# Kernel optimization log

Measured on AMD Instinct MI355X. Metric: run time of the kernel, lower is better.

Reference implementation:

```python
import jax, jax.numpy as jnp
import numpy as np

N_NODES = 50000
N_EDGES = 800000
IN_DIM = 64
EDGE_DIM = 16
HID = 128
L = 3
G = 128  # number of graphs in the batch
EPS = 1e-5


def _glorot(key, shape):
    fan_in, fan_out = shape[0], shape[1]
    lim = float(np.sqrt(6.0 / (fan_in + fan_out)))
    return jax.random.uniform(key, shape, jnp.float32, -lim, lim)


def setup_inputs() -> dict:
    key = jax.random.key(0)
    ks = jax.random.split(key, 40)
    inp = {}
    inp["x"] = jax.random.uniform(ks[0], (N_NODES, IN_DIM), jnp.float32)
    inp["edge_index"] = jax.random.randint(ks[1], (2, N_EDGES), 0, N_NODES, jnp.int64)
    inp["edge_attr"] = jax.random.normal(ks[2], (N_EDGES, EDGE_DIM), jnp.float32)
    inp["batch"] = jnp.sort(jax.random.randint(ks[3], (N_NODES,), 0, G, jnp.int64))
    # ligand / protein input MLPs: Linear-ReLU-Linear-ReLU
    inp["lig_w1"] = _glorot(ks[4], (IN_DIM, HID)); inp["lig_b1"] = jnp.zeros((HID,), jnp.float32)
    inp["lig_w2"] = _glorot(ks[5], (HID, HID));    inp["lig_b2"] = jnp.zeros((HID,), jnp.float32)
    inp["prot_w1"] = _glorot(ks[6], (IN_DIM, HID)); inp["prot_b1"] = jnp.zeros((HID,), jnp.float32)
    inp["prot_w2"] = _glorot(ks[7], (HID, HID));    inp["prot_b2"] = jnp.zeros((HID,), jnp.float32)
    # per-layer GINEConv params (stacked over layers)
    inp["edge_w"] = jnp.stack([_glorot(ks[8 + i], (EDGE_DIM, HID)) for i in range(L)])
    inp["edge_b"] = jnp.zeros((L, HID), jnp.float32)
    inp["nn_w1"] = jnp.stack([_glorot(ks[12 + i], (HID, HID)) for i in range(L)])
    inp["nn_b1"] = jnp.zeros((L, HID), jnp.float32)
    inp["nn_w2"] = jnp.stack([_glorot(ks[16 + i], (HID, HID)) for i in range(L)])
    inp["nn_b2"] = jnp.zeros((L, HID), jnp.float32)
    # GraphNorm params: weight=1, bias=0, mean_scale=1
    inp["gn_w"] = jnp.ones((L, HID), jnp.float32)
    inp["gn_b"] = jnp.zeros((L, HID), jnp.float32)
    inp["gn_ms"] = jnp.ones((L, HID), jnp.float32)
    # output head: Linear-ReLU-Linear(1)
    inp["fc_w1"] = _glorot(ks[20], (HID, HID)); inp["fc_b1"] = jnp.zeros((HID,), jnp.float32)
    inp["fc_w2"] = _glorot(ks[21], (HID, 1));   inp["fc_b2"] = jnp.zeros((1,), jnp.float32)
    return inp


def reference(x, edge_index, edge_attr, batch,
              lig_w1, lig_b1, lig_w2, lig_b2,
              prot_w1, prot_b1, prot_w2, prot_b2,
              edge_w, edge_b, nn_w1, nn_b1, nn_w2, nn_b2,
              gn_w, gn_b, gn_ms,
              fc_w1, fc_b1, fc_w2, fc_b2):
    relu = lambda a: jnp.maximum(a, 0)
    src, dst = edge_index[0], edge_index[1]

    # input encoders, merged per node by protein flag (last feature column)
    is_prot = x[:, -1] > 0.5
    h_lig = relu(relu(x @ lig_w1 + lig_b1) @ lig_w2 + lig_b2)
    h_prot = relu(relu(x @ prot_w1 + prot_b1) @ prot_w2 + prot_b2)
    h = jnp.where(is_prot[:, None], h_prot, h_lig)

    # per-graph node counts for GraphNorm
    cnt = jax.ops.segment_sum(jnp.ones((x.shape[0],), jnp.float32), batch, num_segments=G)
    cnt = jnp.maximum(cnt, 1.0)[:, None]

    for l in range(L):
        # GINEConv (eps=0): out = nn(x + sum_{j->i} relu(x_j + lin(e_ji)))
        e = edge_attr @ edge_w[l] + edge_b[l]              # [E, HID]
        msg = relu(h[src] + e)                             # gather + add + relu
        aggr = jax.ops.segment_sum(msg, dst, num_segments=h.shape[0])
        h = aggr + h
        h = relu(h @ nn_w1[l] + nn_b1[l]) @ nn_w2[l] + nn_b2[l]
        # GraphNorm: per-graph mean/var with learnable mean_scale
        mean = jax.ops.segment_sum(h, batch, num_segments=G) / cnt
        hc = h - mean[batch] * gn_ms[l]
        var = jax.ops.segment_sum(hc * hc, batch, num_segments=G) / cnt
        h = gn_w[l] * hc * jax.lax.rsqrt(var[batch] + EPS) + gn_b[l]
        h = relu(h)  # (dropout=0.0 -> identity)

    g = jax.ops.segment_sum(h, batch, num_segments=G)      # global_add_pool
    out = relu(g @ fc_w1 + fc_b1) @ fc_w2 + fc_b2
    return out.reshape(-1)
```

## Files before the change

### kernel.cpp

```cpp
#include <hip/hip_runtime.h>

#define N_NODES 50000
#define N_EDGES 800000
#define IN_DIM  64
#define EDGE_DIM 16
#define HID     128
#define NLAYERS 3
#define NGRAPH  128
#define EPS     1e-5f

typedef __attribute__((ext_vector_type(8))) short bf8_t;
typedef __attribute__((ext_vector_type(4))) short bf4_t;
typedef __attribute__((ext_vector_type(4))) float f32x4;

__device__ __forceinline__ unsigned short f2bf(float x) {
    unsigned u = __float_as_uint(x);
    unsigned r = u + 0x7fffu + ((u >> 16) & 1u);
    return (unsigned short)(r >> 16);
}
__device__ __forceinline__ float bf2f(unsigned short v) {
    return __uint_as_float(((unsigned)v) << 16);
}

__global__ void k_init(int* __restrict__ row_cnt, float* __restrict__ pool,
                       float* __restrict__ gsum, float* __restrict__ gsq) {
    int i = blockIdx.x * blockDim.x + threadIdx.x;
    if (i < N_NODES) row_cnt[i] = 0;
    if (i < NGRAPH * HID) { pool[i] = 0.0f; gsum[i] = 0.0f; gsq[i] = 0.0f; }
}

__global__ __launch_bounds__(NGRAPH) void k_count(const int* __restrict__ batch,
                                                  float* __restrict__ cnt) {
    int g = threadIdx.x;
    int lo = 0, hi = N_NODES;
    while (lo < hi) { int mid = (lo + hi) >> 1; if (batch[mid] < g) lo = mid + 1; else hi = mid; }
    int a = lo;
    lo = 0; hi = N_NODES;
    while (lo < hi) { int mid = (lo + hi) >> 1; if (batch[mid] < g + 1) lo = mid + 1; else hi = mid; }
    cnt[g] = (float)(lo - a);
}

__global__ void k_wconv(const float* __restrict__ nw1, const float* __restrict__ nw2,
                        unsigned short* __restrict__ wt) {
    int idx = blockIdx.x * 256 + threadIdx.x;
    if (idx >= NLAYERS * 2 * HID * HID) return;
    int k = idx & 127;
    int n = (idx >> 7) & 127;
    int which = (idx >> 14) & 1;
    int l = idx >> 15;
    const float* w = (which == 0 ? nw1 : nw2) + l * HID * HID;
    wt[idx] = f2bf(w[k * HID + n]);
}

__global__ void k_wconv_enc(const float* __restrict__ lw1, const float* __restrict__ pw1,
                            const float* __restrict__ lw2, const float* __restrict__ pw2,
                            unsigned short* __restrict__ we) {
    int idx = blockIdx.x * 256 + threadIdx.x;
    if (idx >= 49152) return;
    float v;
    if (idx < 8192)       { int n = idx >> 6, k = idx & 63;            v = lw1[k * HID + n]; }
    else if (idx < 16384) { int r = idx - 8192;  int n = r >> 6, k = r & 63;  v = pw1[k * HID + n]; }
    else if (idx < 32768) { int r = idx - 16384; int n = r >> 7, k = r & 127; v = lw2[k * HID + n]; }
    else                  { int r = idx - 32768; int n = r >> 7, k = r & 127; v = pw2[k * HID + n]; }
    we[idx] = f2bf(v);
}

__global__ void k_wconv_e(const float* __restrict__ ew, const float* __restrict__ eb,
                          unsigned short* __restrict__ wte) {
    int idx = blockIdx.x * 256 + threadIdx.x;
    if (idx >= NLAYERS * 8 * 64 * 8) return;
    int j = idx & 7;
    int lane = (idx >> 3) & 63;
    int t = (idx >> 9) & 7;
    int l = idx >> 12;
    int k = (lane >> 4) * 8 + j;
    int feat = t * 16 + (lane & 15);
    float v = 0.0f;
    if (k < EDGE_DIM)       v = ew[l * EDGE_DIM * HID + k * HID + feat];
    else if (k == EDGE_DIM) v = eb[l * HID + feat];
    wte[idx] = f2bf(v);
}

__global__ void k_hist(const int* __restrict__ dsts, int* __restrict__ row_cnt) {
    int e = blockIdx.x * blockDim.x + threadIdx.x;
    if (e < N_EDGES) atomicAdd(&row_cnt[dsts[e]], 1);
}

__global__ __launch_bounds__(256) void k_scan1(const int* __restrict__ row_cnt,
                                               int* __restrict__ partial) {
    __shared__ int s[256];
    int t = threadIdx.x, b = blockIdx.x;
    int i0 = b * 512 + t;
    int v = 0;
    if (i0 < N_NODES) v += row_cnt[i0];
    if (i0 + 256 < N_NODES) v += row_cnt[i0 + 256];
    s[t] = v; __syncthreads();
    for (int off = 128; off > 0; off >>= 1) {
        if (t < off) s[t] += s[t + off];
        __syncthreads();
    }
    if (t == 0) partial[b] = s[0];
}

#define NCHUNK 98
__global__ __launch_bounds__(128) void k_scan2(int* __restrict__ partial) {
    __shared__ int s[128];
    int t = threadIdx.x;
    int v = (t < NCHUNK) ? partial[t] : 0;
    s[t] = v; __syncthreads();
    for (int off = 1; off < 128; off <<= 1) {
        int x = (t >= off) ? s[t - off] : 0;
        __syncthreads();
        s[t] += x;
        __syncthreads();
    }
    partial[t] = s[t] - v;
}

__global__ __launch_bounds__(512) void k_scan3(const int* __restrict__ row_cnt,
                                               const int* __restrict__ partial,
                                               int* __restrict__ row_start,
                                               int* __restrict__ row_fill) {
    __shared__ int s[512];
    int t = threadIdx.x, b = blockIdx.x;
    int i = b * 512 + t;
    int v = (i < N_NODES) ? row_cnt[i] : 0;
    s[t] = v; __syncthreads();
    for (int off = 1; off < 512; off <<= 1) {
        int x = (t >= off) ? s[t - off] : 0;
        __syncthreads();
        s[t] += x;
        __syncthreads();
    }
    int excl = s[t] - v + partial[b];
    if (i < N_NODES) { row_start[i] = excl; row_fill[i] = excl; }
}

__global__ void k_fill(const int* __restrict__ srcs, const int* __restrict__ dsts,
                       int* __restrict__ row_fill, int2* __restrict__ csr_se) {
    int e = blockIdx.x * blockDim.x + threadIdx.x;
    if (e < N_EDGES) {
        int p = atomicAdd(&row_fill[dsts[e]], 1);
        csr_se[p] = make_int2(srcs[e], e);
    }
}

__global__ __launch_bounds__(256) void k_reorder(const int2* __restrict__ csr_se,
                                                 const float* __restrict__ ea,
                                                 int* __restrict__ csr_src,
                                                 unsigned short* __restrict__ cea) {
    int p = blockIdx.x * blockDim.x + threadIdx.x;
    if (p < N_EDGES) {
        int2 se = csr_se[p];
        csr_src[p] = se.x;
        const float* s = ea + (size_t)se.y * EDGE_DIM;
        float4 a0 = *(const float4*)(s);
        float4 a1 = *(const float4*)(s + 4);
        float4 a2 = *(const float4*)(s + 8);
        float4 a3 = *(const float4*)(s + 12);
        bf8_t v0, v1;
        v0[0] = (short)f2bf(a0.x); v0[1] = (short)f2bf(a0.y);
        v0[2] = (short)f2bf(a0.z); v0[3] = (short)f2bf(a0.w);
        v0[4] = (short)f2bf(a1.x); v0[5] = (short)f2bf(a1.y);
        v0[6] = (short)f2bf(a1.z); v0[7] = (short)f2bf(a1.w);
        v1[0] = (short)f2bf(a2.x); v1[1] = (short)f2bf(a2.y);
        v1[2] = (short)f2bf(a2.z); v1[3] = (short)f2bf(a2.w);
        v1[4] = (short)f2bf(a3.x); v1[5] = (short)f2bf(a3.y);
        v1[6] = (short)f2bf(a3.z); v1[7] = (short)f2bf(a3.w);
        *(bf8_t*)(cea + (size_t)p * EDGE_DIM) = v0;
        *(bf8_t*)(cea + (size_t)p * EDGE_DIM + 8) = v1;
    }
}

#define HS 136
__global__ __launch_bounds__(256, 8) void k_encoder_mfma(
    const float* __restrict__ x,
    const unsigned short* __restrict__ we,
    const float* __restrict__ lb1, const float* __restrict__ lb2,
    const float* __restrict__ pb1, const float* __restrict__ pb2,
    unsigned short* __restrict__ Hbp) {
    __shared__ short h1s[4][16 * HS];
    int w = threadIdx.x >> 6, lane = threadIdx.x & 63;
    int m = lane & 15, quad = lane >> 4;
    int tile = w >> 1, role = w & 1;
    int nb = blockIdx.x * 32 + tile * 16;
    short* hl = h1s[w];
    int nclamp = nb + m; if (nclamp >= N_NODES) nclamp = N_NODES - 1;
    const float* xp = x + (size_t)nclamp * IN_DIM;
    const float* b1 = role ? pb1 : lb1;
    const float* b2 = role ? pb2 : lb2;
    const unsigned short* w1 = we + role * 8192;
    const unsigned short* w2 = we + 16384 + role * 16384;

    f32x4 a1[8];
    #pragma unroll
    for (int t = 0; t < 8; ++t) {
        float bv = b1[t * 16 + m];
        a1[t] = (f32x4){bv, bv, bv, bv};
    }
    #pragma unroll
    for (int s_ = 0; s_ < 2; ++s_) {
        int k0 = s_ * 32 + quad * 8;
        float4 a0 = *(const float4*)(xp + k0);
        float4 a1v = *(const float4*)(xp + k0 + 4);
        bf8_t af;
        af[0] = (short)f2bf(a0.x); af[1] = (short)f2bf(a0.y);
        af[2] = (short)f2bf(a0.z); af[3] = (short)f2bf(a0.w);
        af[4] = (short)f2bf(a1v.x); af[5] = (short)f2bf(a1v.y);
        af[6] = (short)f2bf(a1v.z); af[7] = (short)f2bf(a1v.w);
        #pragma unroll
        for (int t = 0; t < 8; ++t) {
            bf8_t bw = *(const bf8_t*)(w1 + (t * 16 + m) * 64 + k0);
            a1[t] = __builtin_amdgcn_mfma_f32_16x16x32_bf16(af, bw, a1[t], 0, 0, 0);
        }
    }
    #pragma unroll
    for (int t = 0; t < 8; ++t)
        #pragma unroll
        for (int r = 0; r < 4; ++r)
            hl[(quad * 4 + r) * HS + t * 16 + m] = (short)f2bf(fmaxf(a1[t][r], 0.0f));
    __syncthreads();
    f32x4 a2[8];
    #pragma unroll
    for (int t = 0; t < 8; ++t) {
        float bv = b2[t * 16 + m];
        a2[t] = (f32x4){bv, bv, bv, bv};
    }
    #pragma unroll
    for (int s_ = 0; s_ < 4; ++s_) {
        int k0 = s_ * 32 + quad * 8;
        bf8_t af = *(const bf8_t*)(hl + m * HS + k0);
        #pragma unroll
        for (int t = 0; t < 8; ++t) {
            bf8_t bw = *(const bf8_t*)(w2 + (t * 16 + m) * 128 + k0);
            a2[t] = __builtin_amdgcn_mfma_f32_16x16x32_bf16(af, bw, a2[t], 0, 0, 0);
        }
    }
    #pragma unroll
    for (int r = 0; r < 4; ++r) {
        int node = nb + quad * 4 + r;
        if (node < N_NODES) {
            bool prot = x[(size_t)node * IN_DIM + (IN_DIM - 1)] > 0.5f;
            if (prot == (role == 1)) {
                bf8_t o;
                #pragma unroll
                for (int t = 0; t < 8; ++t)
                    o[t] = (short)f2bf(fmaxf(a2[t][r], 0.0f));
                *(bf8_t*)(Hbp + (size_t)node * HID + m * 8) = o;
            }
        }
    }
}

__global__ __launch_bounds__(256, 8) void k_gather(
    const int* __restrict__ csr_src, const unsigned short* __restrict__ cea,
    const int* __restrict__ row_start, const int* __restrict__ row_end,
    const unsigned short* __restrict__ wte,
    const unsigned short* __restrict__ Hbp, unsigned short* __restrict__ Abp) {
    int w = threadIdx.x >> 6, lane = threadIdx.x & 63;
    int m = lane & 15, quad = lane >> 4;
    int n = blockIdx.x * 2 + (w >> 1);
    int half = w & 1;

    bf8_t bw[4];
    #pragma unroll
    for (int t = 0; t < 4; ++t)
        bw[t] = *(const bf8_t*)(wte + ((size_t)(half * 4 + t) * 64 + lane) * 8);

    float acc[4];
    #pragma unroll
    for (int t = 0; t < 4; ++t) acc[t] = 0.0f;

    int p  = __builtin_amdgcn_readfirstlane(row_start[n]);
    int pe = __builtin_amdgcn_readfirstlane(row_end[n]);

    const f32x4 zc = (f32x4){0.0f, 0.0f, 0.0f, 0.0f};

    for (; p + 16 <= pe; p += 16) {
        bf8_t af = (bf8_t){0, 0, 0, 0, 0, 0, 0, 0};
        if (quad < 2)
            af = *(const bf8_t*)(cea + (size_t)(p + m) * EDGE_DIM + quad * 8);
        else if (quad == 2)
            af[0] = (short)0x3F80;
        int sr[4];
        #pragma unroll
        for (int r = 0; r < 4; ++r) sr[r] = csr_src[p + quad * 4 + r];
        bf4_t hrow[4];
        #pragma unroll
        for (int r = 0; r < 4; ++r)
            hrow[r] = *(const bf4_t*)(Hbp + (size_t)sr[r] * HID + m * 8 + half * 4);
        f32x4 d[4];
        #pragma unroll
        for (int t = 0; t < 4; ++t)
            d[t] = __builtin_amdgcn_mfma_f32_16x16x32_bf16(af, bw[t], zc, 0, 0, 0);
        #pragma unroll
        for (int t = 0; t < 4; ++t)
            #pragma unroll
            for (int r = 0; r < 4; ++r)
                acc[t] += fmaxf(bf2f((unsigned short)hrow[r][t]) + d[t][r], 0.0f);
    }
    int rem = pe - p;
    if (rem > 0) {
        bf8_t af = (bf8_t){0, 0, 0, 0, 0, 0, 0, 0};
        if (quad < 2 && m < rem)
            af = *(const bf8_t*)(cea + (size_t)(p + m) * EDGE_DIM + quad * 8);
        else if (quad == 2)
            af[0] = (short)0x3F80;
        int sr[4];
        #pragma unroll
        for (int r = 0; r < 4; ++r) {
            int idx = p + quad * 4 + r; if (idx >= pe) idx = pe - 1;
            sr[r] = csr_src[idx];
        }
        bf4_t hrow[4];
        #pragma unroll
        for (int r = 0; r < 4; ++r)
            hrow[r] = *(const bf4_t*)(Hbp + (size_t)sr[r] * HID + m * 8 + half * 4);
        f32x4 d[4];
        #pragma unroll
        for (int t = 0; t < 4; ++t)
            d[t] = __builtin_amdgcn_mfma_f32_16x16x32_bf16(af, bw[t], zc, 0, 0, 0);
        #pragma unroll
        for (int t = 0; t < 4; ++t)
            #pragma unroll
            for (int r = 0; r < 4; ++r)
                if (quad * 4 + r < rem)
                    acc[t] += fmaxf(bf2f((unsigned short)hrow[r][t]) + d[t][r], 0.0f);
    }
    #pragma unroll
    for (int t = 0; t < 4; ++t) {
        acc[t] += __shfl_xor(acc[t], 16);
        acc[t] += __shfl_xor(acc[t], 32);
    }
    float asel = (quad == 0) ? acc[0] : (quad == 1) ? acc[1] : (quad == 2) ? acc[2] : acc[3];
    float self_ = bf2f(Hbp[(size_t)n * HID + m * 8 + half * 4 + quad]);
    Abp[(size_t)n * HID + (half * 4 + quad) * 16 + m] = f2bf(asel + self_);
}

#define MLP_NODES_PER_BLOCK 32
__global__ __launch_bounds__(256, 6) void k_mlp_mfma(
    const unsigned short* __restrict__ Abp, const int* __restrict__ batch,
    const unsigned short* __restrict__ wt1, const unsigned short* __restrict__ wt2,
    const float* __restrict__ b1, const float* __restrict__ b2,
    unsigned short* __restrict__ Hb, float* __restrict__ gsum, float* __restrict__ gsq) {
    __shared__ short h1s[2][16 * HS];
    int w = threadIdx.x >> 6;
    int lane = threadIdx.x & 63;
    int m = lane & 15;
    int quad = lane >> 4;
    int tile = w >> 1, role = w & 1;
    int nb = blockIdx.x * MLP_NODES_PER_BLOCK + tile * 16;
    short* hw = h1s[tile];
    int fbase = role * 64;

    int nclamp = nb + m; if (nclamp >= N_NODES) nclamp = N_NODES - 1;
    const unsigned short* Ap = Abp + (size_t)nclamp * HID;
    f32x4 acc1[4];
    #pragma unroll
    for (int t = 0; t < 4; ++t) {
        float bv = b1[fbase + t * 16 + m];
        acc1[t] = (f32x4){bv, bv, bv, bv};
    }
    #pragma unroll
    for (int s_ = 0; s_ < 4; ++s_) {
        int k0 = s_ * 32 + quad * 8;
        bf8_t af = *(const bf8_t*)(Ap + k0);
        #pragma unroll
        for (int t = 0; t < 4; ++t) {
            bf8_t bf = *(const bf8_t*)(wt1 + (size_t)(fbase + t * 16 + m) * HID + k0);
            acc1[t] = __builtin_amdgcn_mfma_f32_16x16x32_bf16(af, bf, acc1[t], 0, 0, 0);
        }
    }
    #pragma unroll
    for (int t = 0; t < 4; ++t)
        #pragma unroll
        for (int r = 0; r < 4; ++r) {
            float v = fmaxf(acc1[t][r], 0.0f);
            hw[(quad * 4 + r) * HS + fbase + t * 16 + m] = (short)f2bf(v);
        }
    __syncthreads();
    f32x4 acc2[4];
    #pragma unroll
    for (int t = 0; t < 4; ++t) {
        float bv = b2[fbase + t * 16 + m];
        acc2[t] = (f32x4){bv, bv, bv, bv};
    }
    #pragma unroll
    for (int s_ = 0; s_ < 4; ++s_) {
        int k0 = s_ * 32 + quad * 8;
        bf8_t af = *(const bf8_t*)(hw + m * HS + k0);
        #pragma unroll
        for (int t = 0; t < 4; ++t) {
            bf8_t bf = *(const bf8_t*)(wt2 + (size_t)(fbase + t * 16 + m) * HID + k0);
            acc2[t] = __builtin_amdgcn_mfma_f32_16x16x32_bf16(af, bf, acc2[t], 0, 0, 0);
        }
    }
    #pragma unroll
    for (int t = 0; t < 4; ++t)
        #pragma unroll
        for (int r = 0; r < 4; ++r) {
            int node = nb + quad * 4 + r;
            if (node < N_NODES) Hb[(size_t)node * HID + fbase + t * 16 + m] = f2bf(acc2[t][r]);
        }
    int blast = nb + 15 < N_NODES ? batch[nb + 15] : -1;
    int g0 = batch[nb < N_NODES ? nb : N_NODES - 1];
    if (nb + 15 < N_NODES && g0 == blast) {
        #pragma unroll
        for (int t = 0; t < 4; ++t) {
            float s = 0.0f, q = 0.0f;
            #pragma unroll
            for (int r = 0; r < 4; ++r) { float v = acc2[t][r]; s += v; q += v * v; }
            s += __shfl_xor(s, 16); q += __shfl_xor(q, 16);
            s += __shfl_xor(s, 32); q += __shfl_xor(q, 32);
            if (quad == 0) {
                atomicAdd(&gsum[g0 * HID + fbase + t * 16 + m], s);
                atomicAdd(&gsq[g0 * HID + fbase + t * 16 + m], q);
            }
        }
    } else {
        #pragma unroll
        for (int t = 0; t < 4; ++t)
            #pragma unroll
            for (int r = 0; r < 4; ++r) {
                int node = nb + quad * 4 + r;
                if (node < N_NODES) {
                    int g = batch[node];
                    float v = acc2[t][r];
                    atomicAdd(&gsum[g * HID + fbase + t * 16 + m], v);
                    atomicAdd(&gsq[g * HID + fbase + t * 16 + m], v * v);
                }
            }
    }
}

__global__ __launch_bounds__(HID) void k_stats(
    float* __restrict__ gsum, float* __restrict__ gsq,
    const float* __restrict__ cnt,
    const float* __restrict__ gw, const float* __restrict__ gb,
    const float* __restrict__ gms,
    float* __restrict__ sc, float* __restrict__ of) {
    int g = blockIdx.x;
    int t = threadIdx.x;
    float c = fmaxf(cnt[g], 1.0f);
    float mean = gsum[g * HID + t] / c;
    float msq  = gsq[g * HID + t] / c;
    float ms = gms[t];
    float var = msq - mean * mean * ms * (2.0f - ms);
    var = fmaxf(var, 0.0f);
    float istd = rsqrtf(var + EPS);
    float s = gw[t] * istd;
    sc[g * HID + t] = s;
    of[g * HID + t] = gb[t] - s * mean * ms;
    gsum[g * HID + t] = 0.0f;
    gsq[g * HID + t]  = 0.0f;
}

#define NORM_N 8
__global__ __launch_bounds__(HID) void k_norm(
    const unsigned short* __restrict__ Hb, const int* __restrict__ batch,
    const float* __restrict__ sc, const float* __restrict__ of,
    unsigned short* __restrict__ Hbp, float* __restrict__ pool, int accumulate) {
    int n0 = blockIdx.x * NORM_N;
    int t = threadIdx.x;
    int m = t & 15, tt = t >> 4;
    int g0 = batch[n0], gN = batch[n0 + NORM_N - 1];
    if (g0 == gN) {
        float ssc = sc[g0 * HID + t], sof = of[g0 * HID + t];
        float ps = 0.0f;
        #pragma unroll
        for (int i = 0; i < NORM_N; ++i) {
            float v = fmaxf(bf2f(Hb[(size_t)(n0 + i) * HID + t]) * ssc + sof, 0.0f);
            Hbp[(size_t)(n0 + i) * HID + m * 8 + tt] = f2bf(v);
            ps += v;
        }
        if (accumulate) atomicAdd(&pool[g0 * HID + t], ps);
    } else {
        #pragma unroll
        for (int i = 0; i < NORM_N; ++i) {
            int g = batch[n0 + i];
            float v = fmaxf(bf2f(Hb[(size_t)(n0 + i) * HID + t]) * sc[g * HID + t] + of[g * HID + t], 0.0f);
            Hbp[(size_t)(n0 + i) * HID + m * 8 + tt] = f2bf(v);
            if (accumulate) atomicAdd(&pool[g * HID + t], v);
        }
    }
}

__global__ __launch_bounds__(HID) void k_head(
    const float* __restrict__ pool,
    const float* __restrict__ fw1, const float* __restrict__ fb1,
    const float* __restrict__ fw2, const float* __restrict__ fb2,
    float* __restrict__ out) {
    __shared__ float ps[HID];
    __shared__ float red[2];
    int g = blockIdx.x;
    int t = threadIdx.x;
    ps[t] = pool[g * HID + t];
    __syncthreads();
    float acc = fb1[t];
    #pragma unroll 4
    for (int k = 0; k < HID; ++k) acc = fmaf(ps[k], fw1[k * HID + t], acc);
    float p = fmaxf(acc, 0.0f) * fw2[t];
    #pragma unroll
    for (int off = 32; off > 0; off >>= 1) p += __shfl_down(p, off, 64);
    if ((t & 63) == 0) red[t >> 6] = p;
    __syncthreads();
    if (t == 0) out[g] = red[0] + red[1] + fb2[0];
}

extern "C" void kernel_launch(void* const* d_in, const int* in_sizes, int n_in,
                              void* d_out, int out_size, void* d_ws, size_t ws_size,
                              hipStream_t stream) {
    const float* x     = (const float*)d_in[0];
    const int*   ei    = (const int*)d_in[1];
    const float* ea    = (const float*)d_in[2];
    const int*   batch = (const int*)d_in[3];
    const float* lw1 = (const float*)d_in[4];
    const float* lb1 = (const float*)d_in[5];
    const float* lw2 = (const float*)d_in[6];
    const float* lb2 = (const float*)d_in[7];
    const float* pw1 = (const float*)d_in[8];
    const float* pb1 = (const float*)d_in[9];
    const float* pw2 = (const float*)d_in[10];
    const float* pb2 = (const float*)d_in[11];
    const float* ew  = (const float*)d_in[12];
    const float* eb  = (const float*)d_in[13];
    const float* nw1 = (const float*)d_in[14];
    const float* nb1 = (const float*)d_in[15];
    const float* nw2 = (const float*)d_in[16];
    const float* nb2 = (const float*)d_in[17];
    const float* gw  = (const float*)d_in[18];
    const float* gb  = (const float*)d_in[19];
    const float* gms = (const float*)d_in[20];
    const float* fw1 = (const float*)d_in[21];
    const float* fb1 = (const float*)d_in[22];
    const float* fw2 = (const float*)d_in[23];
    const float* fb2 = (const float*)d_in[24];
    float* out = (float*)d_out;

    float* ws   = (float*)d_ws;
    float* H    = ws;
    float* A    = H    + (size_t)N_NODES * HID;
    float* gsum = A    + (size_t)N_NODES * HID;
    float* gsq  = gsum + NGRAPH * HID;
    float* sc   = gsq  + NGRAPH * HID;
    float* of   = sc   + NGRAPH * HID;
    float* pool = of   + NGRAPH * HID;
    float* cnt  = pool + NGRAPH * HID;
    int* row_cnt   = (int*)(cnt + NGRAPH);
    int* row_start = row_cnt + N_NODES;
    int* row_fill  = row_start + N_NODES;
    int* partial   = row_fill + N_NODES;
    int* csr_src   = partial + 128;
    unsigned short* cea  = (unsigned short*)(csr_src + N_EDGES);
    unsigned short* wt   = cea + (size_t)N_EDGES * EDGE_DIM;
    unsigned short* wenc = wt + NLAYERS * 2 * HID * HID;
    unsigned short* wte  = wenc + 49152;
    unsigned short* Hbp  = wte + NLAYERS * 8 * 64 * 8;
    unsigned short* Hb   = (unsigned short*)H;
    unsigned short* Abp  = (unsigned short*)A;
    int2* csr_se = (int2*)(Abp + (size_t)N_NODES * HID);

    const int* srcs = ei;
    const int* dsts = ei + N_EDGES;

    k_init<<<(N_NODES + 255) / 256, 256, 0, stream>>>(row_cnt, pool, gsum, gsq);
    k_count<<<1, NGRAPH, 0, stream>>>(batch, cnt);
    k_wconv<<<(NLAYERS * 2 * HID * HID + 255) / 256, 256, 0, stream>>>(nw1, nw2, wt);
    k_wconv_enc<<<(49152 + 255) / 256, 256, 0, stream>>>(lw1, pw1, lw2, pw2, wenc);
    k_wconv_e<<<(NLAYERS * 8 * 64 * 8 + 255) / 256, 256, 0, stream>>>(ew, eb, wte);
    k_hist<<<(N_EDGES + 255) / 256, 256, 0, stream>>>(dsts, row_cnt);
    k_scan1<<<NCHUNK, 256, 0, stream>>>(row_cnt, partial);
    k_scan2<<<1, 128, 0, stream>>>(partial);
    k_scan3<<<NCHUNK, 512, 0, stream>>>(row_cnt, partial, row_start, row_fill);
    k_fill<<<(N_EDGES + 255) / 256, 256, 0, stream>>>(srcs, dsts, row_fill, csr_se);
    k_reorder<<<(N_EDGES + 255) / 256, 256, 0, stream>>>(csr_se, ea, csr_src, cea);

    k_encoder_mfma<<<(N_NODES + 31) / 32, 256, 0, stream>>>(
        x, wenc, lb1, lb2, pb1, pb2, Hbp);

    int mlp_blocks = (N_NODES + MLP_NODES_PER_BLOCK - 1) / MLP_NODES_PER_BLOCK;
    for (int l = 0; l < NLAYERS; ++l) {
        k_gather<<<N_NODES / 2, 256, 0, stream>>>(
            csr_src, cea, row_start, row_fill,
            wte + (size_t)l * 4096, Hbp, Abp);
        k_mlp_mfma<<<mlp_blocks, 256, 0, stream>>>(
            Abp, batch,
            wt + (size_t)l * 2 * HID * HID,
            wt + (size_t)l * 2 * HID * HID + HID * HID,
            nb1 + l * HID, nb2 + l * HID, Hb, gsum, gsq);
        k_stats<<<NGRAPH, HID, 0, stream>>>(gsum, gsq, cnt,
                                            gw + l * HID, gb + l * HID, gms + l * HID,
                                            sc, of);
        k_norm<<<N_NODES / NORM_N, HID, 0, stream>>>(
            Hb, batch, sc, of, Hbp, pool, (l == NLAYERS - 1) ? 1 : 0);
    }
    k_head<<<NGRAPH, HID, 0, stream>>>(pool, fw1, fb1, fw2, fb2, out);
}
```

Baseline: 659.2 us.

## Fuse edge gather with node MLP and fold GraphNorm stats into norm kernel

Merges the per-layer gather kernel and the two-layer MLP kernel into one kernel. It processes 16 nodes per block, keeps the aggregated features in shared memory instead of writing and re-reading an Abp buffer, and splits the MLP output columns across four waves. The separate stats kernel is removed. Per-layer gsum/gsq buffers are zeroed once up front, and k_norm recomputes scale and offset inline. This cuts global traffic and two launches per layer, but each block now runs 8 serial gather tasks per wave, so per-block latency and load imbalance may increase.

```diff
diff --git a/kernel.cpp b/kernel.cpp
--- a/kernel.cpp
+++ b/kernel.cpp
@@ -26,7 +26,8 @@
                        float* __restrict__ gsum, float* __restrict__ gsq) {
     int i = blockIdx.x * blockDim.x + threadIdx.x;
     if (i < N_NODES) row_cnt[i] = 0;
-    if (i < NGRAPH * HID) { pool[i] = 0.0f; gsum[i] = 0.0f; gsq[i] = 0.0f; }
+    if (i < NGRAPH * HID) pool[i] = 0.0f;
+    if (i < NLAYERS * NGRAPH * HID) { gsum[i] = 0.0f; gsq[i] = 0.0f; }
 }
 
 __global__ __launch_bounds__(NGRAPH) void k_count(const int* __restrict__ batch,
@@ -252,161 +253,150 @@
     }
 }
 
-__global__ __launch_bounds__(256, 8) void k_gather(
+#define GM_NODES 16
+__global__ __launch_bounds__(256, 8) void k_gm(
     const int* __restrict__ csr_src, const unsigned short* __restrict__ cea,
     const int* __restrict__ row_start, const int* __restrict__ row_end,
     const unsigned short* __restrict__ wte,
-    const unsigned short* __restrict__ Hbp, unsigned short* __restrict__ Abp) {
-    int w = threadIdx.x >> 6, lane = threadIdx.x & 63;
-    int m = lane & 15, quad = lane >> 4;
-    int n = blockIdx.x * 2 + (w >> 1);
-    int half = w & 1;
-
-    bf8_t bw[4];
-    #pragma unroll
-    for (int t = 0; t < 4; ++t)
-        bw[t] = *(const bf8_t*)(wte + ((size_t)(half * 4 + t) * 64 + lane) * 8);
-
-    float acc[4];
-    #pragma unroll
-    for (int t = 0; t < 4; ++t) acc[t] = 0.0f;
-
-    int p  = __builtin_amdgcn_readfirstlane(row_start[n]);
-    int pe = __builtin_amdgcn_readfirstlane(row_end[n]);
-
-    const f32x4 zc = (f32x4){0.0f, 0.0f, 0.0f, 0.0f};
-
-    for (; p + 16 <= pe; p += 16) {
-        bf8_t af = (bf8_t){0, 0, 0, 0, 0, 0, 0, 0};
-        if (quad < 2)
-            af = *(const bf8_t*)(cea + (size_t)(p + m) * EDGE_DIM + quad * 8);
-        else if (quad == 2)
-            af[0] = (short)0x3F80;
-        int sr[4];
-        #pragma unroll
-        for (int r = 0; r < 4; ++r) sr[r] = csr_src[p + quad * 4 + r];
-        bf4_t hrow[4];
-        #pragma unroll
-        for (int r = 0; r < 4; ++r)
-            hrow[r] = *(const bf4_t*)(Hbp + (size_t)sr[r] * HID + m * 8 + half * 4);
-        f32x4 d[4];
-        #pragma unroll
-        for (int t = 0; t < 4; ++t)
-            d[t] = __builtin_amdgcn_mfma_f32_16x16x32_bf16(af, bw[t], zc, 0, 0, 0);
-        #pragma unroll
-        for (int t = 0; t < 4; ++t)
-            #pragma unroll
-            for (int r = 0; r < 4; ++r)
-                acc[t] += fmaxf(bf2f((unsigned short)hrow[r][t]) + d[t][r], 0.0f);
-    }
-    int rem = pe - p;
-    if (rem > 0) {
-        bf8_t af = (bf8_t){0, 0, 0, 0, 0, 0, 0, 0};
-        if (quad < 2 && m < rem)
-            af = *(const bf8_t*)(cea + (size_t)(p + m) * EDGE_DIM + quad * 8);
-        else if (quad == 2)
-            af[0] = (short)0x3F80;
-        int sr[4];
-        #pragma unroll
-        for (int r = 0; r < 4; ++r) {
-            int idx = p + quad * 4 + r; if (idx >= pe) idx = pe - 1;
-            sr[r] = csr_src[idx];
-        }
-        bf4_t hrow[4];
-        #pragma unroll
-        for (int r = 0; r < 4; ++r)
-            hrow[r] = *(const bf4_t*)(Hbp + (size_t)sr[r] * HID + m * 8 + half * 4);
-        f32x4 d[4];
-        #pragma unroll
-        for (int t = 0; t < 4; ++t)
-            d[t] = __builtin_amdgcn_mfma_f32_16x16x32_bf16(af, bw[t], zc, 0, 0, 0);
-        #pragma unroll
-        for (int t = 0; t < 4; ++t)
-            #pragma unroll
-            for (int r = 0; r < 4; ++r)
-                if (quad * 4 + r < rem)
-                    acc[t] += fmaxf(bf2f((unsigned short)hrow[r][t]) + d[t][r], 0.0f);
-    }
-    #pragma unroll
-    for (int t = 0; t < 4; ++t) {
-        acc[t] += __shfl_xor(acc[t], 16);
-        acc[t] += __shfl_xor(acc[t], 32);
-    }
-    float asel = (quad == 0) ? acc[0] : (quad == 1) ? acc[1] : (quad == 2) ? acc[2] : acc[3];
-    float self_ = bf2f(Hbp[(size_t)n * HID + m * 8 + half * 4 + quad]);
-    Abp[(size_t)n * HID + (half * 4 + quad) * 16 + m] = f2bf(asel + self_);
-}
-
-#define MLP_NODES_PER_BLOCK 32
-__global__ __launch_bounds__(256, 6) void k_mlp_mfma(
-    const unsigned short* __restrict__ Abp, const int* __restrict__ batch,
+    const unsigned short* __restrict__ Hbp, const int* __restrict__ batch,
     const unsigned short* __restrict__ wt1, const unsigned short* __restrict__ wt2,
     const float* __restrict__ b1, const float* __restrict__ b2,
     unsigned short* __restrict__ Hb, float* __restrict__ gsum, float* __restrict__ gsq) {
-    __shared__ short h1s[2][16 * HS];
-    int w = threadIdx.x >> 6;
-    int lane = threadIdx.x & 63;
-    int m = lane & 15;
-    int quad = lane >> 4;
-    int tile = w >> 1, role = w & 1;
-    int nb = blockIdx.x * MLP_NODES_PER_BLOCK + tile * 16;
-    short* hw = h1s[tile];
-    int fbase = role * 64;
-
-    int nclamp = nb + m; if (nclamp >= N_NODES) nclamp = N_NODES - 1;
-    const unsigned short* Ap = Abp + (size_t)nclamp * HID;
-    f32x4 acc1[4];
-    #pragma unroll
-    for (int t = 0; t < 4; ++t) {
+    __shared__ short Als[GM_NODES * HS];
+    __shared__ short h1s[GM_NODES * HS];
+    int w = threadIdx.x >> 6, lane = threadIdx.x & 63;
+    int m = lane & 15, quad = lane >> 4;
+    int nb = blockIdx.x * GM_NODES;
+
+    const f32x4 zc = (f32x4){0.0f, 0.0f, 0.0f, 0.0f};
+
+    for (int task = 0; task < 8; ++task) {
+        int nl = w * 4 + (task >> 1);
+        int half = task & 1;
+        int n = nb + nl;
+
+        bf8_t bw[4];
+        #pragma unroll
+        for (int t = 0; t < 4; ++t)
+            bw[t] = *(const bf8_t*)(wte + ((size_t)(half * 4 + t) * 64 + lane) * 8);
+
+        float acc[4];
+        #pragma unroll
+        for (int t = 0; t < 4; ++t) acc[t] = 0.0f;
+
+        int p  = __builtin_amdgcn_readfirstlane(row_start[n]);
+        int pe = __builtin_amdgcn_readfirstlane(row_end[n]);
+
+        for (; p + 16 <= pe; p += 16) {
+            bf8_t af = (bf8_t){0, 0, 0, 0, 0, 0, 0, 0};
+            if (quad < 2)
+                af = *(const bf8_t*)(cea + (size_t)(p + m) * EDGE_DIM + quad * 8);
+            else if (quad == 2)
+                af[0] = (short)0x3F80;
+            int sr[4];
+            #pragma unroll
+            for (int r = 0; r < 4; ++r) sr[r] = csr_src[p + quad * 4 + r];
+            bf4_t hrow[4];
+            #pragma unroll
+            for (int r = 0; r < 4; ++r)
+                hrow[r] = *(const bf4_t*)(Hbp + (size_t)sr[r] * HID + m * 8 + half * 4);
+            #pragma unroll
+            for (int t = 0; t < 4; ++t) {
+                f32x4 d = __builtin_amdgcn_mfma_f32_16x16x32_bf16(af, bw[t], zc, 0, 0, 0);
+                #pragma unroll
+                for (int r = 0; r < 4; ++r)
+                    acc[t] += fmaxf(bf2f((unsigned short)hrow[r][t]) + d[r], 0.0f);
+            }
+        }
+        int rem = pe - p;
+        if (rem > 0) {
+            bf8_t af = (bf8_t){0, 0, 0, 0, 0, 0, 0, 0};
+            if (quad < 2 && m < rem)
+                af = *(const bf8_t*)(cea + (size_t)(p + m) * EDGE_DIM + quad * 8);
+            else if (quad == 2)
+                af[0] = (short)0x3F80;
+            int sr[4];
+            #pragma unroll
+            for (int r = 0; r < 4; ++r) {
+                int idx = p + quad * 4 + r; if (idx >= pe) idx = pe - 1;
+                sr[r] = csr_src[idx];
+            }
+            bf4_t hrow[4];
+            #pragma unroll
+            for (int r = 0; r < 4; ++r)
+                hrow[r] = *(const bf4_t*)(Hbp + (size_t)sr[r] * HID + m * 8 + half * 4);
+            #pragma unroll
+            for (int t = 0; t < 4; ++t) {
+                f32x4 d = __builtin_amdgcn_mfma_f32_16x16x32_bf16(af, bw[t], zc, 0, 0, 0);
+                #pragma unroll
+                for (int r = 0; r < 4; ++r)
+                    if (quad * 4 + r < rem)
+                        acc[t] += fmaxf(bf2f((unsigned short)hrow[r][t]) + d[r], 0.0f);
+            }
+        }
+        #pragma unroll
+        for (int t = 0; t < 4; ++t) {
+            acc[t] += __shfl_xor(acc[t], 16);
+            acc[t] += __shfl_xor(acc[t], 32);
+        }
+        float asel = (quad == 0) ? acc[0] : (quad == 1) ? acc[1] : (quad == 2) ? acc[2] : acc[3];
+        float self_ = bf2f(Hbp[(size_t)n * HID + m * 8 + half * 4 + quad]);
+        Als[nl * HS + (half * 4 + quad) * 16 + m] = (short)f2bf(asel + self_);
+    }
+    __syncthreads();
+
+    int fbase = w * 32;
+    f32x4 acc1[2];
+    #pragma unroll
+    for (int t = 0; t < 2; ++t) {
         float bv = b1[fbase + t * 16 + m];
         acc1[t] = (f32x4){bv, bv, bv, bv};
     }
     #pragma unroll
     for (int s_ = 0; s_ < 4; ++s_) {
         int k0 = s_ * 32 + quad * 8;
-        bf8_t af = *(const bf8_t*)(Ap + k0);
-        #pragma unroll
-        for (int t = 0; t < 4; ++t) {
+        bf8_t af = *(const bf8_t*)(Als + m * HS + k0);
+        #pragma unroll
+        for (int t = 0; t < 2; ++t) {
             bf8_t bf = *(const bf8_t*)(wt1 + (size_t)(fbase + t * 16 + m) * HID + k0);
             acc1[t] = __builtin_amdgcn_mfma_f32_16x16x32_bf16(af, bf, acc1[t], 0, 0, 0);
         }
     }
     #pragma unroll
-    for (int t = 0; t < 4; ++t)
+    for (int t = 0; t < 2; ++t)
         #pragma unroll
         for (int r = 0; r < 4; ++r) {
             float v = fmaxf(acc1[t][r], 0.0f);
-            hw[(quad * 4 + r) * HS + fbase + t * 16 + m] = (short)f2bf(v);
+            h1s[(quad * 4 + r) * HS + fbase + t * 16 + m] = (short)f2bf(v);
         }
     __syncthreads();
-    f32x4 acc2[4];
-    #pragma unroll
-    for (int t = 0; t < 4; ++t) {
+    f32x4 acc2[2];
+    #pragma unroll
+    for (int t = 0; t < 2; ++t) {
         float bv = b2[fbase + t * 16 + m];
         acc2[t] = (f32x4){bv, bv, bv, bv};
     }
     #pragma unroll
     for (int s_ = 0; s_ < 4; ++s_) {
         int k0 = s_ * 32 + quad * 8;
-        bf8_t af = *(const bf8_t*)(hw + m * HS + k0);
-        #pragma unroll
-        for (int t = 0; t < 4; ++t) {
+        bf8_t af = *(const bf8_t*)(h1s + m * HS + k0);
+        #pragma unroll
+        for (int t = 0; t < 2; ++t) {
             bf8_t bf = *(const bf8_t*)(wt2 + (size_t)(fbase + t * 16 + m) * HID + k0);
             acc2[t] = __builtin_amdgcn_mfma_f32_16x16x32_bf16(af, bf, acc2[t], 0, 0, 0);
         }
     }
     #pragma unroll
-    for (int t = 0; t < 4; ++t)
+    for (int t = 0; t < 2; ++t)
         #pragma unroll
         for (int r = 0; r < 4; ++r) {
             int node = nb + quad * 4 + r;
-            if (node < N_NODES) Hb[(size_t)node * HID + fbase + t * 16 + m] = f2bf(acc2[t][r]);
-        }
-    int blast = nb + 15 < N_NODES ? batch[nb + 15] : -1;
-    int g0 = batch[nb < N_NODES ? nb : N_NODES - 1];
-    if (nb + 15 < N_NODES && g0 == blast) {
-        #pragma unroll
-        for (int t = 0; t < 4; ++t) {
+            Hb[(size_t)node * HID + fbase + t * 16 + m] = f2bf(acc2[t][r]);
+        }
+    int g0 = batch[nb];
+    if (batch[nb + 15] == g0) {
+        #pragma unroll
+        for (int t = 0; t < 2; ++t) {
             float s = 0.0f, q = 0.0f;
             #pragma unroll
             for (int r = 0; r < 4; ++r) { float v = acc2[t][r]; s += v; q += v * v; }
@@ -419,53 +409,38 @@
         }
     } else {
         #pragma unroll
-        for (int t = 0; t < 4; ++t)
+        for (int t = 0; t < 2; ++t)
             #pragma unroll
             for (int r = 0; r < 4; ++r) {
                 int node = nb + quad * 4 + r;
-                if (node < N_NODES) {
-                    int g = batch[node];
-                    float v = acc2[t][r];
-                    atomicAdd(&gsum[g * HID + fbase + t * 16 + m], v);
-                    atomicAdd(&gsq[g * HID + fbase + t * 16 + m], v * v);
-                }
+                int g = batch[node];
+                float v = acc2[t][r];
+                atomicAdd(&gsum[g * HID + fbase + t * 16 + m], v);
+                atomicAdd(&gsq[g * HID + fbase + t * 16 + m], v * v);
             }
     }
 }
 
-__global__ __launch_bounds__(HID) void k_stats(
-    float* __restrict__ gsum, float* __restrict__ gsq,
+#define NORM_N 8
+__global__ __launch_bounds__(HID) void k_norm(
+    const unsigned short* __restrict__ Hb, const int* __restrict__ batch,
+    const float* __restrict__ gsum, const float* __restrict__ gsq,
     const float* __restrict__ cnt,
     const float* __restrict__ gw, const float* __restrict__ gb,
     const float* __restrict__ gms,
-    float* __restrict__ sc, float* __restrict__ of) {
-    int g = blockIdx.x;
-    int t = threadIdx.x;
-    float c = fmaxf(cnt[g], 1.0f);
-    float mean = gsum[g * HID + t] / c;
-    float msq  = gsq[g * HID + t] / c;
-    float ms = gms[t];
-    float var = msq - mean * mean * ms * (2.0f - ms);
-    var = fmaxf(var, 0.0f);
-    float istd = rsqrtf(var + EPS);
-    float s = gw[t] * istd;
-    sc[g * HID + t] = s;
-    of[g * HID + t] = gb[t] - s * mean * ms;
-    gsum[g * HID + t] = 0.0f;
-    gsq[g * HID + t]  = 0.0f;
-}
-
-#define NORM_N 8
-__global__ __launch_bounds__(HID) void k_norm(
-    const unsigned short* __restrict__ Hb, const int* __restrict__ batch,
-    const float* __restrict__ sc, const float* __restrict__ of,
     unsigned short* __restrict__ Hbp, float* __restrict__ pool, int accumulate) {
     int n0 = blockIdx.x * NORM_N;
     int t = threadIdx.x;
     int m = t & 15, tt = t >> 4;
+    float ms = gms[t], gwt = gw[t], gbt = gb[t];
     int g0 = batch[n0], gN = batch[n0 + NORM_N - 1];
     if (g0 == gN) {
-        float ssc = sc[g0 * HID + t], sof = of[g0 * HID + t];
+        float c = fmaxf(cnt[g0], 1.0f);
+        float mean = gsum[g0 * HID + t] / c;
+        float msq  = gsq[g0 * HID + t] / c;
+        float var = fmaxf(msq - mean * mean * ms * (2.0f - ms), 0.0f);
+        float ssc = gwt * rsqrtf(var + EPS);
+        float sof = gbt - ssc * mean * ms;
         float ps = 0.0f;
         #pragma unroll
         for (int i = 0; i < NORM_N; ++i) {
@@ -478,7 +453,13 @@
         #pragma unroll
         for (int i = 0; i < NORM_N; ++i) {
             int g = batch[n0 + i];
-            float v = fmaxf(bf2f(Hb[(size_t)(n0 + i) * HID + t]) * sc[g * HID + t] + of[g * HID + t], 0.0f);
+            float c = fmaxf(cnt[g], 1.0f);
+            float mean = gsum[g * HID + t] / c;
+            float msq  = gsq[g * HID + t] / c;
+            float var = fmaxf(msq - mean * mean * ms * (2.0f - ms), 0.0f);
+            float ssc = gwt * rsqrtf(var + EPS);
+            float sof = gbt - ssc * mean * ms;
+            float v = fmaxf(bf2f(Hb[(size_t)(n0 + i) * HID + t]) * ssc + sof, 0.0f);
             Hbp[(size_t)(n0 + i) * HID + m * 8 + tt] = f2bf(v);
             if (accumulate) atomicAdd(&pool[g * HID + t], v);
         }
@@ -541,10 +522,8 @@
     float* H    = ws;
     float* A    = H    + (size_t)N_NODES * HID;
     float* gsum = A    + (size_t)N_NODES * HID;
-    float* gsq  = gsum + NGRAPH * HID;
-    float* sc   = gsq  + NGRAPH * HID;
-    float* of   = sc   + NGRAPH * HID;
-    float* pool = of   + NGRAPH * HID;
+    float* gsq  = gsum + NLAYERS * NGRAPH * HID;
+    float* pool = gsq  + NLAYERS * NGRAPH * HID;
     float* cnt  = pool + NGRAPH * HID;
     int* row_cnt   = (int*)(cnt + NGRAPH);
     int* row_start = row_cnt + N_NODES;
@@ -557,8 +536,7 @@
     unsigned short* wte  = wenc + 49152;
     unsigned short* Hbp  = wte + NLAYERS * 8 * 64 * 8;
     unsigned short* Hb   = (unsigned short*)H;
-    unsigned short* Abp  = (unsigned short*)A;
-    int2* csr_se = (int2*)(Abp + (size_t)N_NODES * HID);
+    int2* csr_se = (int2*)(((unsigned short*)A) + (size_t)N_NODES * HID);
 
     const int* srcs = ei;
     const int* dsts = ei + N_EDGES;
@@ -578,21 +556,19 @@
     k_encoder_mfma<<<(N_NODES + 31) / 32, 256, 0, stream>>>(
         x, wenc, lb1, lb2, pb1, pb2, Hbp);
 
-    int mlp_blocks = (N_NODES + MLP_NODES_PER_BLOCK - 1) / MLP_NODES_PER_BLOCK;
     for (int l = 0; l < NLAYERS; ++l) {
-        k_gather<<<N_NODES / 2, 256, 0, stream>>>(
+        k_gm<<<N_NODES / GM_NODES, 256, 0, stream>>>(
             csr_src, cea, row_start, row_fill,
-            wte + (size_t)l * 4096, Hbp, Abp);
-        k_mlp_mfma<<<mlp_blocks, 256, 0, stream>>>(
-            Abp, batch,
+            wte + (size_t)l * 4096, Hbp, batch,
             wt + (size_t)l * 2 * HID * HID,
             wt + (size_t)l * 2 * HID * HID + HID * HID,
-            nb1 + l * HID, nb2 + l * HID, Hb, gsum, gsq);
-        k_stats<<<NGRAPH, HID, 0, stream>>>(gsum, gsq, cnt,
-                                            gw + l * HID, gb + l * HID, gms + l * HID,
-                                            sc, of);
+            nb1 + l * HID, nb2 + l * HID,
+            Hb, gsum + (size_t)l * NGRAPH * HID, gsq + (size_t)l * NGRAPH * HID);
         k_norm<<<N_NODES / NORM_N, HID, 0, stream>>>(
-            Hb, batch, sc, of, Hbp, pool, (l == NLAYERS - 1) ? 1 : 0);
+            Hb, batch,
+            gsum + (size_t)l * NGRAPH * HID, gsq + (size_t)l * NGRAPH * HID,
+            cnt, gw + l * HID, gb + l * HID, gms + l * HID,
+            Hbp, pool, (l == NLAYERS - 1) ? 1 : 0);
     }
     k_head<<<NGRAPH, HID, 0, stream>>>(pool, fw1, fb1, fw2, fb2, out);
 }
```

Result: no change. 669.8 us (+1.6%).
